# Kernel tuning notes

Hardware: AMD Instinct MI355X
Metric: run time of the kernel (lower is better)

## Reference

```python
import jax, jax.numpy as jnp
import numpy as np

NUM_SKILLS = 1000
DIM_S = 64
SIZE_M = 64
B, T = 64, 200


def setup_inputs() -> dict:
    key = jax.random.key(0)
    ks = jax.random.split(key, 16)
    skills = jax.random.randint(ks[0], (B, T), 0, NUM_SKILLS)
    responses = jax.random.randint(ks[1], (B, T), 0, 2)
    s = 1.0 / np.sqrt(DIM_S)
    return {
        "skills": skills,
        "responses": responses,
        "k_emb": jax.random.normal(ks[2], (NUM_SKILLS, DIM_S)) * s,
        "v_emb": jax.random.normal(ks[3], (2 * NUM_SKILLS, DIM_S)) * s,
        "Mk": jax.random.normal(ks[4], (SIZE_M, DIM_S)) * np.sqrt(2.0 / DIM_S),
        "Mv0": jax.random.normal(ks[5], (SIZE_M, DIM_S)) * np.sqrt(2.0 / DIM_S),
        "fW": jax.random.normal(ks[6], (DIM_S, 2 * DIM_S)) * (1.0 / np.sqrt(2 * DIM_S)),
        "fb": jnp.zeros((DIM_S,)),
        "eW": jax.random.normal(ks[7], (DIM_S, DIM_S)) * s,
        "eb": jnp.zeros((DIM_S,)),
        "aW": jax.random.normal(ks[8], (DIM_S, DIM_S)) * s,
        "ab": jnp.zeros((DIM_S,)),
        "pW": jax.random.normal(ks[9], (1, DIM_S)) * s,
        "pb": jnp.zeros((1,)),
    }


def reference(skills, responses, k_emb, v_emb, Mk, Mv0, fW, fb, eW, eb, aW, ab, pW, pb):
    # dropout is identity in eval mode
    masked_r = responses * (responses > -1).astype(responses.dtype)
    x = skills + NUM_SKILLS * masked_r            # [B, T]
    k = k_emb[skills]                              # [B, T, D]
    v = v_emb[x]                                   # [B, T, D]
    w = jax.nn.softmax(jnp.einsum('btd,md->btm', k, Mk), axis=-1)  # [B, T, M]
    e = jax.nn.sigmoid(v @ eW.T + eb)              # [B, T, D]
    a = jnp.tanh(v @ aW.T + ab)                    # [B, T, D]

    Mv_init = jnp.broadcast_to(Mv0, (skills.shape[0],) + Mv0.shape)  # [B, M, D]

    def step(Mvt, inp):
        wt, et, at = inp                           # [B,M], [B,D], [B,D]
        read = jnp.einsum('bm,bmd->bd', wt, Mvt)   # read BEFORE update (Mv[:, :-1])
        Mvt = Mvt * (1.0 - wt[:, :, None] * et[:, None, :]) + wt[:, :, None] * at[:, None, :]
        return Mvt, read

    xs = (jnp.swapaxes(w, 0, 1), jnp.swapaxes(e, 0, 1), jnp.swapaxes(a, 0, 1))
    _, reads = jax.lax.scan(step, Mv_init, xs)     # reads: [T, B, D]
    reads = jnp.swapaxes(reads, 0, 1)              # [B, T, D]

    f = jnp.tanh(jnp.concatenate([reads, k], axis=-1) @ fW.T + fb)  # [B, T, D]
    p = jax.nn.sigmoid(f @ pW.T + pb)[..., 0]      # [B, T]
    return p[:, 1:]                                # pred, [B, T-1]
```

## Files before the change

### kernel.cpp

```cpp
#include <hip/hip_runtime.h>
#include <stdint.h>

#define NSK 1000
#define TT  200
#define BB  64
#define NROW (BB * TT)
#define NOUT (BB * (TT-1))
#define CH  10
#define RW  1
#define NSPLIT 16
#define PSTR ((size_t)NROW * 64)

__device__ __forceinline__ float frcp(float x) { return __builtin_amdgcn_rcpf(x); }
__device__ __forceinline__ float sigm(float x) { return frcp(1.f + __expf(-x)); }
__device__ __forceinline__ float tanh_fast(float x) {
  return fmaf(-2.f, frcp(1.f + __expf(2.f * x)), 1.f);
}

typedef _Float16 half2v __attribute__((ext_vector_type(2)));
typedef _Float16 v8h __attribute__((ext_vector_type(8)));
typedef float    v4f __attribute__((ext_vector_type(4)));
union H2U { unsigned u; half2v h; };
union V8U { uint4 u; v8h h; };
__device__ __forceinline__ unsigned pack2h(float a, float b) {
  H2U x; x.h = (half2v){(_Float16)a, (_Float16)b}; return x.u;
}
__device__ __forceinline__ unsigned short f16bits(float x) {
  H2U u; u.h = (half2v){(_Float16)x, (_Float16)0.f}; return (unsigned short)(u.u & 0xffffu);
}
__device__ __forceinline__ float f16lo(unsigned bits) {
  H2U u; u.u = bits; return (float)u.h.x;
}
__device__ __forceinline__ float f16hi(unsigned bits) {
  H2U u; u.u = bits; return (float)u.h.y;
}
__device__ __forceinline__ v8h pk8(float4 x0, float4 x1) {
  return (v8h){(_Float16)x0.x, (_Float16)x0.y, (_Float16)x0.z, (_Float16)x0.w,
               (_Float16)x1.x, (_Float16)x1.y, (_Float16)x1.z, (_Float16)x1.w};
}

__global__ __launch_bounds__(128) void wea_mfma(
    const int* __restrict__ skills, const int* __restrict__ responses,
    const float* __restrict__ k_emb, const float* __restrict__ v_emb,
    const float* __restrict__ Mk, const float* __restrict__ eW,
    const float* __restrict__ eb, const float* __restrict__ aW,
    const float* __restrict__ ab,
    unsigned* __restrict__ ea_ws, unsigned short* __restrict__ w16_ws)
{
  const int tid  = threadIdx.x;
  const int wv   = tid >> 6, lane = tid & 63;
  const int tile = blockIdx.x * 2 + wv;
  const int r0   = tile * 16;
  const int lr   = lane & 15;
  const int lg   = lane >> 4;

  const int sk = skills[r0 + lr];
  int rr = responses[r0 + lr]; rr = (rr > -1) ? rr : 0;
  const int vrow = sk + NSK * rr;

  const float4* kq = (const float4*)(k_emb + (size_t)sk * 64);
  const float4* vq = (const float4*)(v_emb + (size_t)vrow * 64);
  v8h ak[2], av[2];
  #pragma unroll
  for (int t = 0; t < 2; ++t) {
    const int o = t * 8 + lg * 2;
    ak[t] = pk8(kq[o], kq[o + 1]);
    av[t] = pk8(vq[o], vq[o + 1]);
  }

  float ebv[4], abv[4];
  #pragma unroll
  for (int c = 0; c < 4; ++c) { ebv[c] = eb[16 * c + lr]; abv[c] = ab[16 * c + lr]; }

  v4f acK[4], acE[4], acA[4];
  #pragma unroll
  for (int c = 0; c < 4; ++c) {
    acK[c] = (v4f){0.f, 0.f, 0.f, 0.f};
    acE[c] = (v4f){0.f, 0.f, 0.f, 0.f};
    acA[c] = (v4f){0.f, 0.f, 0.f, 0.f};
  }

  #pragma unroll
  for (int c = 0; c < 4; ++c) {
    const float4* mq = (const float4*)(Mk + (size_t)(16 * c + lr) * 64);
    const float4* eq = (const float4*)(eW + (size_t)(16 * c + lr) * 64);
    const float4* aq = (const float4*)(aW + (size_t)(16 * c + lr) * 64);
    #pragma unroll
    for (int t = 0; t < 2; ++t) {
      const int o = t * 8 + lg * 2;
      const v8h bm = pk8(mq[o], mq[o + 1]);
      const v8h be = pk8(eq[o], eq[o + 1]);
      const v8h ba = pk8(aq[o], aq[o + 1]);
      acK[c] = __builtin_amdgcn_mfma_f32_16x16x32_f16(ak[t], bm, acK[c], 0, 0, 0);
      acE[c] = __builtin_amdgcn_mfma_f32_16x16x32_f16(av[t], be, acE[c], 0, 0, 0);
      acA[c] = __builtin_amdgcn_mfma_f32_16x16x32_f16(av[t], ba, acA[c], 0, 0, 0);
    }
  }

  float rs[4];
  #pragma unroll
  for (int q = 0; q < 4; ++q) {
    float m = fmaxf(fmaxf(acK[0][q], acK[1][q]), fmaxf(acK[2][q], acK[3][q]));
    #pragma unroll
    for (int off = 8; off; off >>= 1) m = fmaxf(m, __shfl_xor(m, off));
    float s = 0.f;
    #pragma unroll
    for (int c = 0; c < 4; ++c) {
      acK[c][q] = __expf(acK[c][q] - m);
      s += acK[c][q];
    }
    #pragma unroll
    for (int off = 8; off; off >>= 1) s += __shfl_xor(s, off);
    rs[q] = frcp(s);
  }

  #pragma unroll
  for (int c = 0; c < 4; ++c) {
    const int j = 16 * c + lr;
    #pragma unroll
    for (int q = 0; q < 4; ++q) {
      const int row = r0 + lg * 4 + q;
      w16_ws[(size_t)row * 64 + j] = f16bits(acK[c][q] * rs[q]);
      const float ev = sigm(acE[c][q] + ebv[c]);
      const float avv = tanh_fast(acA[c][q] + abv[c]);
      ea_ws[(size_t)row * 64 + j] = pack2h(ev, avv);
    }
  }
}

__global__ __launch_bounds__(256) void scan_kernel(
    const float* __restrict__ Mv0,
    const unsigned* __restrict__ ea_ws, const unsigned short* __restrict__ w16_ws,
    unsigned short* __restrict__ pbase)
{
  __shared__ float red[2][CH * 256];
  const int b    = blockIdx.x >> 4;
  const int s    = blockIdx.x & 15;
  const int wave = threadIdx.x >> 6;
  const int lane = threadIdx.x & 63;
  const size_t base = (size_t)b * TT;
  const int m0   = s * 4 + wave;
  unsigned short* ps = pbase + (size_t)s * PSTR;

  float Mv = Mv0[(size_t)m0 * 64 + lane];

  const unsigned* eap = ea_ws + base * 64;
  const unsigned short* wp = w16_ws + base * 64;

  unsigned ea0[CH], wv0[CH], ea1[CH], wv1[CH];
  #pragma unroll
  for (int k = 0; k < CH; ++k) {
    ea0[k] = eap[k * 64 + lane];
    wv0[k] = (unsigned)wp[k * 64 + m0];
  }
  for (int ch = 0; ch < TT / CH; ch += 2) {
    #pragma unroll
    for (int k = 0; k < CH; ++k) {
      ea1[k] = eap[((ch + 1) * CH + k) * 64 + lane];
      wv1[k] = (unsigned)wp[((ch + 1) * CH + k) * 64 + m0];
    }
    #pragma unroll
    for (int k = 0; k < CH; ++k) {
      const float ev = f16lo(ea0[k]), av = f16hi(ea0[k]);
      const float wm = f16lo(wv0[k]);
      red[0][k * 256 + wave * 64 + lane] = wm * Mv;
      Mv = fmaf(wm, fmaf(-ev, Mv, av), Mv);
    }
    __syncthreads();
    for (int k = wave; k < CH; k += 4) {
      const float* rr = red[0] + k * 256;
      const float v = (rr[lane] + rr[64 + lane]) + (rr[128 + lane] + rr[192 + lane]);
      ps[(base + ch * CH + k) * 64 + lane] = f16bits(v);
    }
    if ((ch + 2) * CH < TT) {
      #pragma unroll
      for (int k = 0; k < CH; ++k) {
        ea0[k] = eap[((ch + 2) * CH + k) * 64 + lane];
        wv0[k] = (unsigned)wp[((ch + 2) * CH + k) * 64 + m0];
      }
    }
    #pragma unroll
    for (int k = 0; k < CH; ++k) {
      const float ev = f16lo(ea1[k]), av = f16hi(ea1[k]);
      const float wm = f16lo(wv1[k]);
      red[1][k * 256 + wave * 64 + lane] = wm * Mv;
      Mv = fmaf(wm, fmaf(-ev, Mv, av), Mv);
    }
    __syncthreads();
    for (int k = wave; k < CH; k += 4) {
      const float* rr = red[1] + k * 256;
      const float v = (rr[lane] + rr[64 + lane]) + (rr[128 + lane] + rr[192 + lane]);
      ps[(base + (ch + 1) * CH + k) * 64 + lane] = f16bits(v);
    }
  }
}

__global__ __launch_bounds__(256) void fp_mfma(
    const int* __restrict__ skills, const float* __restrict__ k_emb,
    const float* __restrict__ fW, const float* __restrict__ fb,
    const float* __restrict__ pW, const float* __restrict__ pb,
    const unsigned short* __restrict__ pbase,
    float* __restrict__ out)
{
  const int tid  = threadIdx.x;
  const int wv   = tid >> 6, lane = tid & 63;
  const int lr   = lane & 15;
  const int lg   = lane >> 4;
  const int o0   = (blockIdx.x * 4 + wv) * 16;

  const unsigned idx = o0 + lr;
  const unsigned bb  = idx / 199u;
  const unsigned t2  = idx - bb * 199u;
  const int srow     = (int)(idx + bb + 1u);

  v8h ar[4];
  #pragma unroll
  for (int t = 0; t < 2; ++t) {
    const size_t eo = (size_t)srow * 64 + t * 32 + lg * 8;
    v8h g[4];
    #pragma unroll
    for (int pp = 0; pp < 4; ++pp) {
      V8U s0, s1, s2, s3;
      s0.u = *(const uint4*)&pbase[eo + (size_t)(4 * pp) * PSTR];
      s1.u = *(const uint4*)&pbase[eo + (size_t)(4 * pp + 1) * PSTR];
      s2.u = *(const uint4*)&pbase[eo + (size_t)(4 * pp + 2) * PSTR];
      s3.u = *(const uint4*)&pbase[eo + (size_t)(4 * pp + 3) * PSTR];
      g[pp] = (s0.h + s1.h) + (s2.h + s3.h);
    }
    ar[t] = (g[0] + g[1]) + (g[2] + g[3]);
  }
  {
    const float4* kq = (const float4*)(k_emb + (size_t)skills[srow] * 64);
    #pragma unroll
    for (int t = 2; t < 4; ++t) {
      const int o = (t - 2) * 8 + lg * 2;
      ar[t] = pk8(kq[o], kq[o + 1]);
    }
  }

  float fbv[4], pwv[4];
  #pragma unroll
  for (int c = 0; c < 4; ++c) { fbv[c] = fb[16 * c + lr]; pwv[c] = pW[16 * c + lr]; }

  v4f acc[4];
  #pragma unroll
  for (int c = 0; c < 4; ++c) acc[c] = (v4f){0.f, 0.f, 0.f, 0.f};

  const float4* fq = (const float4*)fW;
  #pragma unroll
  for (int c = 0; c < 4; ++c) {
    const int jb = (16 * c + lr) * 32;
    #pragma unroll
    for (int t = 0; t < 4; ++t) {
      const int o = jb + t * 8 + lg * 2;
      const v8h bf = pk8(fq[o], fq[o + 1]);
      acc[c] = __builtin_amdgcn_mfma_f32_16x16x32_f16(ar[t], bf, acc[c], 0, 0, 0);
    }
  }

  const float pb0 = pb[0];
  #pragma unroll
  for (int q = 0; q < 4; ++q) {
    float s = 0.f;
    #pragma unroll
    for (int c = 0; c < 4; ++c)
      s += tanh_fast(acc[c][q] + fbv[c]) * pwv[c];
    #pragma unroll
    for (int off = 8; off; off >>= 1) s += __shfl_xor(s, off);
    if (lr == lg * 4 + q)
      out[(size_t)bb * (TT - 1) + t2] = sigm(s + pb0);
  }
}

extern "C" void kernel_launch(void* const* d_in, const int* in_sizes, int n_in,
                              void* d_out, int out_size, void* d_ws, size_t ws_size,
                              hipStream_t stream) {
  const int* skills    = (const int*)d_in[0];
  const int* responses = (const int*)d_in[1];
  const float* k_emb   = (const float*)d_in[2];
  const float* v_emb   = (const float*)d_in[3];
  const float* Mk      = (const float*)d_in[4];
  const float* Mv0     = (const float*)d_in[5];
  const float* fW      = (const float*)d_in[6];
  const float* fb      = (const float*)d_in[7];
  const float* eW      = (const float*)d_in[8];
  const float* eb      = (const float*)d_in[9];
  const float* aW      = (const float*)d_in[10];
  const float* ab      = (const float*)d_in[11];
  const float* pW      = (const float*)d_in[12];
  const float* pb      = (const float*)d_in[13];
  (void)in_sizes; (void)n_in; (void)out_size; (void)ws_size;

  unsigned* ea_ws        = (unsigned*)d_ws;
  unsigned short* w16_ws = (unsigned short*)(ea_ws + (size_t)NROW * 64);
  unsigned short* pbase  = w16_ws + PSTR;

  wea_mfma<<<dim3(400), 128, 0, stream>>>(
      skills, responses, k_emb, v_emb, Mk, eW, eb, aW, ab, ea_ws, w16_ws);
  scan_kernel<<<dim3(BB * NSPLIT), 256, 0, stream>>>(Mv0, ea_ws, w16_ws, pbase);
  fp_mfma<<<dim3(199), 256, 0, stream>>>(
      skills, k_emb, fW, fb, pW, pb, pbase, (float*)d_out);
}
```

Before: 127.6 us.

## Give each scan wave four memory rows and drop LDS reduction barriers

The scan kernel now assigns four memory slots to each wave, keeping four Mv values in registers and reducing the read across them in-lane. The per-slot weights are broadcast with readlane, which removes the shared-memory reduction and the __syncthreads per chunk. The grid shrinks from 1024 to 256 blocks and the chunk size doubles, giving more serial work per wave and more register pressure, with less parallelism left to hide latency. The partial-read output layout (16 splits) stays the same, so fp_mfma still sums 16 partials.

```diff
diff --git a/kernel.cpp b/kernel.cpp
--- a/kernel.cpp
+++ b/kernel.cpp
@@ -5,12 +5,13 @@
 #define TT  200
 #define BB  64
 #define NROW (BB * TT)
-#define NOUT (BB * (TT-1))
-#define CH  10
-#define RW  1
+#define CH  20
 #define NSPLIT 16
 #define PSTR ((size_t)NROW * 64)
 
+__device__ __forceinline__ unsigned ulane_bcast(unsigned v, int l) {
+  return __builtin_amdgcn_readlane(v, l);
+}
 __device__ __forceinline__ float frcp(float x) { return __builtin_amdgcn_rcpf(x); }
 __device__ __forceinline__ float sigm(float x) { return frcp(1.f + __expf(-x)); }
 __device__ __forceinline__ float tanh_fast(float x) {
@@ -128,21 +129,23 @@
   }
 }
 
-__global__ __launch_bounds__(256) void scan_kernel(
+__global__ __launch_bounds__(256) void scan_nolds(
     const float* __restrict__ Mv0,
     const unsigned* __restrict__ ea_ws, const unsigned short* __restrict__ w16_ws,
     unsigned short* __restrict__ pbase)
 {
-  __shared__ float red[2][CH * 256];
-  const int b    = blockIdx.x >> 4;
-  const int s    = blockIdx.x & 15;
-  const int wave = threadIdx.x >> 6;
+  const int b    = blockIdx.x >> 2;
+  const int sblk = blockIdx.x & 3;
+  const int wv   = threadIdx.x >> 6;
   const int lane = threadIdx.x & 63;
+  const int s16  = sblk * 4 + wv;
+  const int m0   = s16 * 4;
+  unsigned short* ps = pbase + (size_t)s16 * PSTR;
   const size_t base = (size_t)b * TT;
-  const int m0   = s * 4 + wave;
-  unsigned short* ps = pbase + (size_t)s * PSTR;
-
-  float Mv = Mv0[(size_t)m0 * 64 + lane];
+
+  float Mv[4];
+  #pragma unroll
+  for (int i = 0; i < 4; ++i) Mv[i] = Mv0[(size_t)(m0 + i) * 64 + lane];
 
   const unsigned* eap = ea_ws + base * 64;
   const unsigned short* wp = w16_ws + base * 64;
@@ -151,46 +154,45 @@
   #pragma unroll
   for (int k = 0; k < CH; ++k) {
     ea0[k] = eap[k * 64 + lane];
-    wv0[k] = (unsigned)wp[k * 64 + m0];
-  }
+    wv0[k] = (unsigned)wp[k * 64 + m0 + (lane & 3)];
+  }
+  #pragma unroll 1
   for (int ch = 0; ch < TT / CH; ch += 2) {
     #pragma unroll
     for (int k = 0; k < CH; ++k) {
       ea1[k] = eap[((ch + 1) * CH + k) * 64 + lane];
-      wv1[k] = (unsigned)wp[((ch + 1) * CH + k) * 64 + m0];
+      wv1[k] = (unsigned)wp[((ch + 1) * CH + k) * 64 + m0 + (lane & 3)];
     }
     #pragma unroll
     for (int k = 0; k < CH; ++k) {
       const float ev = f16lo(ea0[k]), av = f16hi(ea0[k]);
-      const float wm = f16lo(wv0[k]);
-      red[0][k * 256 + wave * 64 + lane] = wm * Mv;
-      Mv = fmaf(wm, fmaf(-ev, Mv, av), Mv);
-    }
-    __syncthreads();
-    for (int k = wave; k < CH; k += 4) {
-      const float* rr = red[0] + k * 256;
-      const float v = (rr[lane] + rr[64 + lane]) + (rr[128 + lane] + rr[192 + lane]);
-      ps[(base + ch * CH + k) * 64 + lane] = f16bits(v);
+      float rp = 0.f;
+      #pragma unroll
+      for (int i = 0; i < 4; ++i) {
+        const float wm = f16lo(ulane_bcast(wv0[k], i));
+        rp = fmaf(wm, Mv[i], rp);
+        Mv[i] = fmaf(wm, fmaf(-ev, Mv[i], av), Mv[i]);
+      }
+      ps[(base + ch * CH + k) * 64 + lane] = f16bits(rp);
     }
     if ((ch + 2) * CH < TT) {
       #pragma unroll
       for (int k = 0; k < CH; ++k) {
         ea0[k] = eap[((ch + 2) * CH + k) * 64 + lane];
-        wv0[k] = (unsigned)wp[((ch + 2) * CH + k) * 64 + m0];
+        wv0[k] = (unsigned)wp[((ch + 2) * CH + k) * 64 + m0 + (lane & 3)];
       }
     }
     #pragma unroll
     for (int k = 0; k < CH; ++k) {
       const float ev = f16lo(ea1[k]), av = f16hi(ea1[k]);
-      const float wm = f16lo(wv1[k]);
-      red[1][k * 256 + wave * 64 + lane] = wm * Mv;
-      Mv = fmaf(wm, fmaf(-ev, Mv, av), Mv);
-    }
-    __syncthreads();
-    for (int k = wave; k < CH; k += 4) {
-      const float* rr = red[1] + k * 256;
-      const float v = (rr[lane] + rr[64 + lane]) + (rr[128 + lane] + rr[192 + lane]);
-      ps[(base + (ch + 1) * CH + k) * 64 + lane] = f16bits(v);
+      float rp = 0.f;
+      #pragma unroll
+      for (int i = 0; i < 4; ++i) {
+        const float wm = f16lo(ulane_bcast(wv1[k], i));
+        rp = fmaf(wm, Mv[i], rp);
+        Mv[i] = fmaf(wm, fmaf(-ev, Mv[i], av), Mv[i]);
+      }
+      ps[(base + (ch + 1) * CH + k) * 64 + lane] = f16bits(rp);
     }
   }
 }
@@ -297,7 +299,7 @@
 
   wea_mfma<<<dim3(400), 128, 0, stream>>>(
       skills, responses, k_emb, v_emb, Mk, eW, eb, aW, ab, ea_ws, w16_ws);
-  scan_kernel<<<dim3(BB * NSPLIT), 256, 0, stream>>>(Mv0, ea_ws, w16_ws, pbase);
+  scan_nolds<<<dim3(BB * 4), 256, 0, stream>>>(Mv0, ea_ws, w16_ws, pbase);
   fp_mfma<<<dim3(199), 256, 0, stream>>>(
       skills, k_emb, fW, fb, pW, pb, pbase, (float*)d_out);
 }
```

Result: faster. 122.3 us (-4.1%).
